# Kernel tuning notes

Hardware: AMD Instinct MI355X
Metric: run time of the kernel (lower is better)

The kernel has to match this reference:

```python
import jax, jax.numpy as jnp
import numpy as np
from jax import lax


def haar_dwt2(x):
    """Level-1 Haar (db1) 2D DWT on [N, H, W] with even H, W.
    Returns cA, cH, cV (cD is discarded by the module), each [N, H//2, W//2].
    Matches pywt/ptwt db1 block form: cA=(a+b+c+d)/2, etc."""
    a = x[:, 0::2, 0::2]
    b = x[:, 0::2, 1::2]
    c = x[:, 1::2, 0::2]
    d = x[:, 1::2, 1::2]
    cA = (a + b + c + d) * 0.5
    cH = (a + b - c - d) * 0.5  # horizontal detail (highpass along rows axis)
    cV = (a - b + c - d) * 0.5  # vertical detail (highpass along cols axis)
    return cA, cH, cV


def conv2d_same(x, w, b):
    # x: [N, Cin, H, W], w: [Cout, Cin, kh, kw]
    y = lax.conv_general_dilated(x, w, window_strides=(1, 1), padding='SAME',
                                 dimension_numbers=('NCHW', 'OIHW', 'NCHW'))
    return y + b[None, :, None, None]


def maxpool2(x):
    return lax.reduce_window(x, -jnp.inf, lax.max,
                             window_dimensions=(1, 1, 2, 2),
                             window_strides=(1, 1, 2, 2), padding='VALID')


def setup_inputs() -> dict:
    key = jax.random.key(0)
    ks = jax.random.split(key, 7)
    B, C, H, W = 32, 3, 512, 512
    x = jax.random.normal(ks[0], (B, C, H, W), dtype=jnp.float32)
    # conv stack params (Conv2d(1,16,3), Conv2d(16,8,3), Conv2d(8,4,1))
    w1 = jax.random.normal(ks[1], (16, 1, 3, 3), dtype=jnp.float32) * (1.0 / 3.0)
    b1 = jnp.zeros((16,), dtype=jnp.float32)
    w2 = jax.random.normal(ks[2], (8, 16, 3, 3), dtype=jnp.float32) * (1.0 / 12.0)
    b2 = jnp.zeros((8,), dtype=jnp.float32)
    w3 = jax.random.normal(ks[3], (4, 8, 1, 1), dtype=jnp.float32) * (1.0 / 2.83)
    b3 = jnp.zeros((4,), dtype=jnp.float32)
    return {"x": x, "w1": w1, "b1": b1, "w2": w2, "b2": b2, "w3": w3, "b3": b3}


def reference(x, w1, b1, w2, b2, w3, b3):
    B, C, H, W = x.shape
    # Batch the per-image/per-channel loop: treat each channel as one map.
    flat = x.reshape(B * C, H, W)
    cA, cH, cV = haar_dwt2(flat)  # [B*C, H/2, W/2]

    # Low-frequency conv stack on approx coeffs (1 input channel per map).
    h = cA[:, None, :, :]                       # [B*C, 1, H/2, W/2]
    h = maxpool2(jax.nn.relu(conv2d_same(h, w1, b1)))
    h = maxpool2(jax.nn.relu(conv2d_same(h, w2, b2)))
    h = conv2d_same(h, w3, b3)                  # [B*C, 4, H/8, W/8]
    # per-channel flatten, then concat over channels (dim=1 in the original)
    low = h.reshape(B, 1, -1)                   # [B, 1, C*4*(H/8)*(W/8)]

    # High-frequency: per channel concat [cH.flatten(), cV.flatten()],
    # then concat over channels.
    n = (H // 2) * (W // 2)
    high = jnp.concatenate([cH.reshape(B, C, n), cV.reshape(B, C, n)], axis=-1)
    high = high.reshape(B, 1, C * 2 * n)        # [B, 1, C*2*(H/2)*(W/2)]
    return low, high
```

## Files before the change

### kernel.cpp

```cpp
#include <hip/hip_runtime.h>


typedef float v2f __attribute__((ext_vector_type(2)));

#define PK_FMA_W0(acc, w, d) \
    asm("v_pk_fma_f32 %0, %1, %2, %0 op_sel:[0,0,0] op_sel_hi:[1,0,1]" \
        : "+v"(acc) : "s"(w), "v"(d))
#define PK_FMA_W1(acc, w, d) \
    asm("v_pk_fma_f32 %0, %1, %2, %0 op_sel:[0,1,0] op_sel_hi:[1,1,1]" \
        : "+v"(acc) : "s"(w), "v"(d))
#define PK_MUL_W0(dst, w, d) \
    asm("v_pk_mul_f32 %0, %1, %2 op_sel:[0,0] op_sel_hi:[1,0]" \
        : "=v"(dst) : "s"(w), "v"(d))
#define PK_MUL_W1(dst, w, d) \
    asm("v_pk_mul_f32 %0, %1, %2 op_sel:[0,1] op_sel_hi:[1,1]" \
        : "=v"(dst) : "s"(w), "v"(d))

__global__ __launch_bounds__(256, 6) void fused_all_kernel(
    const float* __restrict__ x,
    const float* __restrict__ w1, const float* __restrict__ b1,
    const float* __restrict__ w2, const float* __restrict__ b2,
    const float* __restrict__ w3, const float* __restrict__ b3,
    float* __restrict__ outLow, float* __restrict__ outHigh)
{
    __shared__ __align__(16) float ca[38 * 72];
    __shared__ __align__(16) float h1s[4 * 18 * 36];

    int img = blockIdx.x >> 5;
    int t   = blockIdx.x & 31;
    int tyy = t >> 2, txx = t & 3;
    int hy0 = tyy * 16 - 1, hx0 = txx * 32 - 1;
    int cy0 = tyy * 32 - 3, cx0 = txx * 64 - 3;

    const float* xi = x + img * 262144;
    float* hb = outHigh + img * 131072;

    #pragma unroll
    for (int k = 0; k < 2; ++k) {
        int i = threadIdx.x + k * 256;
        int row = i >> 4, cg = i & 15;
        int gy = tyy * 32 + row;
        int gx = txx * 64 + cg * 4;
        const float* r0 = xi + (2 * gy) * 512 + 2 * gx;
        const float* r1 = r0 + 512;
        float4 t0 = *(const float4*)(r0);
        float4 t1 = *(const float4*)(r0 + 4);
        float4 u0 = *(const float4*)(r1);
        float4 u1 = *(const float4*)(r1 + 4);
        float4 vA, vH, vV;
        vA.x = (t0.x + t0.y + u0.x + u0.y) * 0.5f;
        vH.x = (t0.x + t0.y - u0.x - u0.y) * 0.5f;
        vV.x = (t0.x - t0.y + u0.x - u0.y) * 0.5f;
        vA.y = (t0.z + t0.w + u0.z + u0.w) * 0.5f;
        vH.y = (t0.z + t0.w - u0.z - u0.w) * 0.5f;
        vV.y = (t0.z - t0.w + u0.z - u0.w) * 0.5f;
        vA.z = (t1.x + t1.y + u1.x + u1.y) * 0.5f;
        vH.z = (t1.x + t1.y - u1.x - u1.y) * 0.5f;
        vV.z = (t1.x - t1.y + u1.x - u1.y) * 0.5f;
        vA.w = (t1.z + t1.w + u1.z + u1.w) * 0.5f;
        vH.w = (t1.z + t1.w - u1.z - u1.w) * 0.5f;
        vV.w = (t1.z - t1.w + u1.z - u1.w) * 0.5f;
        int po = (gy << 8) + gx;
        *(float4*)(hb + po) = vH;
        *(float4*)(hb + 65536 + po) = vV;
        float* cp = ca + (row + 3) * 72 + cg * 4 + 3;
        cp[0] = vA.x; cp[1] = vA.y; cp[2] = vA.z; cp[3] = vA.w;
    }

    for (int i = threadIdx.x; i < 612; i += 256) {
        int r, c;
        if (i < 210)      { r = i / 70;              c = i - r * 70; }
        else if (i < 420) { int j = i - 210; r = 35 + j / 70; c = j - (j / 70) * 70; }
        else              { int j = i - 420; r = 3 + j / 6; int k6 = j - (j / 6) * 6;
                            c = (k6 < 3) ? k6 : (64 + k6); }
        int gy = cy0 + r, gx = cx0 + c;
        float v = 0.f;
        if ((unsigned)gy < 256u && (unsigned)gx < 256u) {
            const float* p0 = xi + (2 * gy) * 512 + 2 * gx;
            float2 a = *(const float2*)(p0);
            float2 b = *(const float2*)(p0 + 512);
            v = (a.x + a.y + b.x + b.y) * 0.5f;
        }
        ca[r * 72 + c] = v;
    }

    int pos = threadIdx.x & 127;
    int ocg = __builtin_amdgcn_readfirstlane(threadIdx.x >> 7);
    int ly = pos >> 4, lx = pos & 15;

    v2f acc2[2][2][2];
    #pragma unroll
    for (int o2 = 0; o2 < 2; ++o2)
        #pragma unroll
        for (int r = 0; r < 2; ++r)
            #pragma unroll
            for (int c = 0; c < 2; ++c) acc2[o2][r][c] = (v2f){0.f, 0.f};

    __syncthreads();

    #pragma unroll 1
    for (int cc = 0; cc < 4; ++cc) {
        v2f wp1[2][9];
        #pragma unroll
        for (int o2 = 0; o2 < 2; ++o2)
            #pragma unroll
            for (int k = 0; k < 9; ++k)
                wp1[o2][k] = (v2f){ w1[(cc * 4 + o2 * 2    ) * 9 + k],
                                    w1[(cc * 4 + o2 * 2 + 1) * 9 + k] };
        if (cc) __syncthreads();

        #pragma unroll 1
        for (int k5 = 0; k5 < 3; ++k5) {
            int i = threadIdx.x + k5 * 256;
            if (i < 612) {
                int hy = i / 34, hx = i - hy * 34;
                const float* pb = ca + (2 * hy) * 72 + 2 * hx;
                v2f pr[4][2];
                #pragma unroll
                for (int r = 0; r < 4; ++r) {
                    pr[r][0] = *(const v2f*)(pb + r * 72);
                    pr[r][1] = *(const v2f*)(pb + r * 72 + 2);
                }
                bool oob = ((unsigned)(hy0 + hy) >= 128u) | ((unsigned)(hx0 + hx) >= 128u);
                v2f am[2][4];
                #pragma unroll
                for (int ky = 0; ky < 3; ++ky)
                #pragma unroll
                for (int kx = 0; kx < 3; ++kx) {
                    #pragma unroll
                    for (int o2 = 0; o2 < 2; ++o2)
                    #pragma unroll
                    for (int dy = 0; dy < 2; ++dy)
                    #pragma unroll
                    for (int dx = 0; dx < 2; ++dx) {
                        v2f d = pr[ky + dy][(kx + dx) >> 1];
                        if (ky == 0 && kx == 0) {
                            if (((kx + dx) & 1) == 0) PK_MUL_W0(am[o2][dy * 2 + dx], wp1[o2][0], d);
                            else                      PK_MUL_W1(am[o2][dy * 2 + dx], wp1[o2][0], d);
                        } else {
                            if (((kx + dx) & 1) == 0) PK_FMA_W0(am[o2][dy * 2 + dx], wp1[o2][ky * 3 + kx], d);
                            else                      PK_FMA_W1(am[o2][dy * 2 + dx], wp1[o2][ky * 3 + kx], d);
                        }
                    }
                }
                #pragma unroll
                for (int o2 = 0; o2 < 2; ++o2) {
                    float mx = fmaxf(fmaxf(am[o2][0].x, am[o2][1].x),
                                     fmaxf(am[o2][2].x, am[o2][3].x));
                    float my = fmaxf(fmaxf(am[o2][0].y, am[o2][1].y),
                                     fmaxf(am[o2][2].y, am[o2][3].y));
                    mx = fmaxf(mx + b1[cc * 4 + o2 * 2    ], 0.f);
                    my = fmaxf(my + b1[cc * 4 + o2 * 2 + 1], 0.f);
                    h1s[((o2 * 2    ) * 18 + hy) * 36 + hx] = oob ? 0.f : mx;
                    h1s[((o2 * 2 + 1) * 18 + hy) * 36 + hx] = oob ? 0.f : my;
                }
            }
        }
        __syncthreads();

        #pragma unroll
        for (int icl = 0; icl < 4; ++icl) {
            const float* base = h1s + (icl * 18 + ly * 2) * 36 + lx * 2;
            v2f wr[4][2];
            #pragma unroll
            for (int r = 0; r < 4; ++r) {
                wr[r][0] = *(const v2f*)(base + r * 36);
                wr[r][1] = *(const v2f*)(base + r * 36 + 2);
            }
            int ic = cc * 4 + icl;
            #pragma unroll
            for (int ky = 0; ky < 3; ++ky)
            #pragma unroll
            for (int kx = 0; kx < 3; ++kx)
            #pragma unroll
            for (int o2 = 0; o2 < 2; ++o2) {
                int oc0 = ocg * 4 + o2 * 2;
                v2f wv = (v2f){ w2[((oc0    ) * 16 + ic) * 9 + ky * 3 + kx],
                                w2[((oc0 + 1) * 16 + ic) * 9 + ky * 3 + kx] };
                #pragma unroll
                for (int r = 0; r < 2; ++r)
                #pragma unroll
                for (int c = 0; c < 2; ++c) {
                    v2f d = wr[r + ky][(c + kx) >> 1];
                    if (((c + kx) & 1) == 0) PK_FMA_W0(acc2[o2][r][c], wv, d);
                    else                     PK_FMA_W1(acc2[o2][r][c], wv, d);
                }
            }
        }
    }

    float h2v[4];
    #pragma unroll
    for (int o2 = 0; o2 < 2; ++o2) {
        float mx = fmaxf(fmaxf(acc2[o2][0][0].x, acc2[o2][0][1].x),
                         fmaxf(acc2[o2][1][0].x, acc2[o2][1][1].x));
        float my = fmaxf(fmaxf(acc2[o2][0][0].y, acc2[o2][0][1].y),
                         fmaxf(acc2[o2][1][0].y, acc2[o2][1][1].y));
        h2v[o2 * 2    ] = fmaxf(mx + b2[ocg * 4 + o2 * 2    ], 0.f);
        h2v[o2 * 2 + 1] = fmaxf(my + b2[ocg * 4 + o2 * 2 + 1], 0.f);
    }
    __syncthreads();
    float* hx2 = h1s;
    #pragma unroll
    for (int j = 0; j < 4; ++j) hx2[pos * 9 + ocg * 4 + j] = h2v[j];
    __syncthreads();

    float hv[8];
    #pragma unroll
    for (int ic = 0; ic < 8; ++ic) hv[ic] = hx2[pos * 9 + ic];
    float* dst = outLow + img * 16384;
    int posg = (tyy * 8 + ly) * 64 + txx * 16 + lx;
    int o3g = ocg;
    #pragma unroll
    for (int jo = 0; jo < 2; ++jo) {
        int oc3 = o3g * 2 + jo;
        float s = b3[oc3];
        #pragma unroll
        for (int ic = 0; ic < 8; ++ic) s += w3[oc3 * 8 + ic] * hv[ic];
        dst[oc3 * 4096 + posg] = s;
    }
}

extern "C" void kernel_launch(void* const* d_in, const int* in_sizes, int n_in,
                              void* d_out, int out_size, void* d_ws, size_t ws_size,
                              hipStream_t stream) {
    const float* x  = (const float*)d_in[0];
    const float* w1 = (const float*)d_in[1];
    const float* b1 = (const float*)d_in[2];
    const float* w2 = (const float*)d_in[3];
    const float* b2 = (const float*)d_in[4];
    const float* w3 = (const float*)d_in[5];
    const float* b3 = (const float*)d_in[6];
    float* out     = (float*)d_out;
    float* outLow  = out;
    float* outHigh = out + 1572864;

    fused_all_kernel<<<3072, 256, 0, stream>>>(x, w1, b1, w2, b2, w3, b3,
                                               outLow, outHigh);
}
```

Baseline: 209.7 us.

## Raise occupancy, shrink LDS pitches, wave-balance halo and conv1 work

Raises the launch-bounds minimum from 6 to 8 blocks per CU. Shrinks the shared-memory row pitches (72→70, 36→34), which lowers LDS use per block and changes bank mapping. Redistributes the halo-fill and conv1 loops so each wave takes a contiguous block of 153 items instead of striding across the whole block. Conv2 weights are now loaded in one batch per input channel before the FMA loop. The tighter register budget for 8 blocks/CU risks spills, and the odd pitches may break 8-byte alignment of the v2f LDS loads.

```diff
diff --git a/kernel.cpp b/kernel.cpp
--- a/kernel.cpp
+++ b/kernel.cpp
@@ -16,15 +16,15 @@
     asm("v_pk_mul_f32 %0, %1, %2 op_sel:[0,1] op_sel_hi:[1,1]" \
         : "=v"(dst) : "s"(w), "v"(d))
 
-__global__ __launch_bounds__(256, 6) void fused_all_kernel(
+__global__ __launch_bounds__(256, 8) void fused_all_kernel(
     const float* __restrict__ x,
     const float* __restrict__ w1, const float* __restrict__ b1,
     const float* __restrict__ w2, const float* __restrict__ b2,
     const float* __restrict__ w3, const float* __restrict__ b3,
     float* __restrict__ outLow, float* __restrict__ outHigh)
 {
-    __shared__ __align__(16) float ca[38 * 72];
-    __shared__ __align__(16) float h1s[4 * 18 * 36];
+    __shared__ __align__(16) float ca[38 * 70];
+    __shared__ __align__(16) float h1s[4 * 18 * 34];
 
     int img = blockIdx.x >> 5;
     int t   = blockIdx.x & 31;
@@ -34,6 +34,9 @@
 
     const float* xi = x + img * 262144;
     float* hb = outHigh + img * 131072;
+
+    int wvi = threadIdx.x >> 6;
+    int lni = threadIdx.x & 63;
 
     #pragma unroll
     for (int k = 0; k < 2; ++k) {
@@ -63,25 +66,29 @@
         int po = (gy << 8) + gx;
         *(float4*)(hb + po) = vH;
         *(float4*)(hb + 65536 + po) = vV;
-        float* cp = ca + (row + 3) * 72 + cg * 4 + 3;
+        float* cp = ca + (row + 3) * 70 + cg * 4 + 3;
         cp[0] = vA.x; cp[1] = vA.y; cp[2] = vA.z; cp[3] = vA.w;
     }
 
-    for (int i = threadIdx.x; i < 612; i += 256) {
-        int r, c;
-        if (i < 210)      { r = i / 70;              c = i - r * 70; }
-        else if (i < 420) { int j = i - 210; r = 35 + j / 70; c = j - (j / 70) * 70; }
-        else              { int j = i - 420; r = 3 + j / 6; int k6 = j - (j / 6) * 6;
-                            c = (k6 < 3) ? k6 : (64 + k6); }
-        int gy = cy0 + r, gx = cx0 + c;
-        float v = 0.f;
-        if ((unsigned)gy < 256u && (unsigned)gx < 256u) {
-            const float* p0 = xi + (2 * gy) * 512 + 2 * gx;
-            float2 a = *(const float2*)(p0);
-            float2 b = *(const float2*)(p0 + 512);
-            v = (a.x + a.y + b.x + b.y) * 0.5f;
+    #pragma unroll
+    for (int j = 0; j < 3; ++j) {
+        if (j < 2 || lni < 25) {
+            int i = wvi * 153 + j * 64 + lni;
+            int r, c;
+            if (i < 210)      { r = i / 70;              c = i - r * 70; }
+            else if (i < 420) { int jj = i - 210; r = 35 + jj / 70; c = jj - (jj / 70) * 70; }
+            else              { int jj = i - 420; r = 3 + jj / 6; int k6 = jj - (jj / 6) * 6;
+                                c = (k6 < 3) ? k6 : (64 + k6); }
+            int gy = cy0 + r, gx = cx0 + c;
+            float v = 0.f;
+            if ((unsigned)gy < 256u && (unsigned)gx < 256u) {
+                const float* p0 = xi + (2 * gy) * 512 + 2 * gx;
+                float2 a = *(const float2*)(p0);
+                float2 b = *(const float2*)(p0 + 512);
+                v = (a.x + a.y + b.x + b.y) * 0.5f;
+            }
+            ca[r * 70 + c] = v;
         }
-        ca[r * 72 + c] = v;
     }
 
     int pos = threadIdx.x & 127;
@@ -110,16 +117,16 @@
         if (cc) __syncthreads();
 
         #pragma unroll 1
-        for (int k5 = 0; k5 < 3; ++k5) {
-            int i = threadIdx.x + k5 * 256;
-            if (i < 612) {
+        for (int j = 0; j < 3; ++j) {
+            if (j < 2 || lni < 25) {
+                int i = wvi * 153 + j * 64 + lni;
                 int hy = i / 34, hx = i - hy * 34;
-                const float* pb = ca + (2 * hy) * 72 + 2 * hx;
+                const float* pb = ca + (2 * hy) * 70 + 2 * hx;
                 v2f pr[4][2];
                 #pragma unroll
                 for (int r = 0; r < 4; ++r) {
-                    pr[r][0] = *(const v2f*)(pb + r * 72);
-                    pr[r][1] = *(const v2f*)(pb + r * 72 + 2);
+                    pr[r][0] = *(const v2f*)(pb + r * 70);
+                    pr[r][1] = *(const v2f*)(pb + r * 70 + 2);
                 }
                 bool oob = ((unsigned)(hy0 + hy) >= 128u) | ((unsigned)(hx0 + hx) >= 128u);
                 v2f am[2][4];
@@ -151,8 +158,8 @@
                                      fmaxf(am[o2][2].y, am[o2][3].y));
                     mx = fmaxf(mx + b1[cc * 4 + o2 * 2    ], 0.f);
                     my = fmaxf(my + b1[cc * 4 + o2 * 2 + 1], 0.f);
-                    h1s[((o2 * 2    ) * 18 + hy) * 36 + hx] = oob ? 0.f : mx;
-                    h1s[((o2 * 2 + 1) * 18 + hy) * 36 + hx] = oob ? 0.f : my;
+                    h1s[((o2 * 2    ) * 18 + hy) * 34 + hx] = oob ? 0.f : mx;
+                    h1s[((o2 * 2 + 1) * 18 + hy) * 34 + hx] = oob ? 0.f : my;
                 }
             }
         }
@@ -160,30 +167,36 @@
 
         #pragma unroll
         for (int icl = 0; icl < 4; ++icl) {
-            const float* base = h1s + (icl * 18 + ly * 2) * 36 + lx * 2;
-            v2f wr[4][2];
-            #pragma unroll
-            for (int r = 0; r < 4; ++r) {
-                wr[r][0] = *(const v2f*)(base + r * 36);
-                wr[r][1] = *(const v2f*)(base + r * 36 + 2);
-            }
             int ic = cc * 4 + icl;
-            #pragma unroll
-            for (int ky = 0; ky < 3; ++ky)
-            #pragma unroll
-            for (int kx = 0; kx < 3; ++kx)
+            v2f wl[2][9];
             #pragma unroll
             for (int o2 = 0; o2 < 2; ++o2) {
                 int oc0 = ocg * 4 + o2 * 2;
-                v2f wv = (v2f){ w2[((oc0    ) * 16 + ic) * 9 + ky * 3 + kx],
-                                w2[((oc0 + 1) * 16 + ic) * 9 + ky * 3 + kx] };
+                #pragma unroll
+                for (int k = 0; k < 9; ++k)
+                    wl[o2][k] = (v2f){ w2[((oc0    ) * 16 + ic) * 9 + k],
+                                       w2[((oc0 + 1) * 16 + ic) * 9 + k] };
+            }
+            const float* base = h1s + (icl * 18 + ly * 2) * 34 + lx * 2;
+            v2f wr[4][2];
+            #pragma unroll
+            for (int r = 0; r < 4; ++r) {
+                wr[r][0] = *(const v2f*)(base + r * 34);
+                wr[r][1] = *(const v2f*)(base + r * 34 + 2);
+            }
+            #pragma unroll
+            for (int ky = 0; ky < 3; ++ky)
+            #pragma unroll
+            for (int kx = 0; kx < 3; ++kx)
+            #pragma unroll
+            for (int o2 = 0; o2 < 2; ++o2) {
                 #pragma unroll
                 for (int r = 0; r < 2; ++r)
                 #pragma unroll
                 for (int c = 0; c < 2; ++c) {
                     v2f d = wr[r + ky][(c + kx) >> 1];
-                    if (((c + kx) & 1) == 0) PK_FMA_W0(acc2[o2][r][c], wv, d);
-                    else                     PK_FMA_W1(acc2[o2][r][c], wv, d);
+                    if (((c + kx) & 1) == 0) PK_FMA_W0(acc2[o2][r][c], wl[o2][ky * 3 + kx], d);
+                    else                     PK_FMA_W1(acc2[o2][r][c], wl[o2][ky * 3 + kx], d);
                 }
             }
         }
```

Result: no change. 208.7 us (-0.5%).
